# Performance work log

Hardware: AMD Instinct MI355X
Metric: run time of the kernel (lower is better)

Reference implementation:

```python
import jax, jax.numpy as jnp
import numpy as np

N, E, H, K = 2000, 512, 8, 32
DH = E // H  # 64
CLAMP = 10000.0
LN_EPS = 1e-5


def _layernorm(x, g, b):
    mu = jnp.mean(x, axis=-1, keepdims=True)
    var = jnp.mean((x - mu) ** 2, axis=-1, keepdims=True)
    return (x - mu) * jax.lax.rsqrt(var + LN_EPS) * g + b


def setup_inputs() -> dict:
    key = jax.random.key(0)
    ks = jax.random.split(key, 16)
    s_in = 1.0 / np.sqrt(E)
    inp = {
        'x': jax.random.normal(ks[0], (N, E), jnp.float32),
        'coords9': jax.random.normal(ks[1], (N, 9), jnp.float32),
        'prompt_signal': jax.random.normal(ks[2], (E,), jnp.float32),
        # pos_encoder: Linear(3, E//4) + GELU + LayerNorm(E//4)
        'pos_w1': jax.random.normal(ks[3], (E // 4, 3), jnp.float32) * 0.5,
        'pos_b1': jax.random.normal(ks[4], (E // 4,), jnp.float32) * 0.02,
        'pos_ln_g': jnp.ones((E // 4,), jnp.float32),
        'pos_ln_b': jnp.zeros((E // 4,), jnp.float32),
        # MultiheadAttention in/out projections
        'wq': jax.random.normal(ks[5], (E, E), jnp.float32) * s_in,
        'wk': jax.random.normal(ks[6], (E, E), jnp.float32) * s_in,
        'wv': jax.random.normal(ks[7], (E, E), jnp.float32) * s_in,
        'bq': jnp.zeros((E,), jnp.float32),
        'bk': jnp.zeros((E,), jnp.float32),
        'bv': jnp.zeros((E,), jnp.float32),
        'wo': jax.random.normal(ks[8], (E, E), jnp.float32) * s_in,
        'bo': jnp.zeros((E,), jnp.float32),
    }
    return inp


def reference(x, coords9, prompt_signal, pos_w1, pos_b1, pos_ln_g, pos_ln_b,
              wq, wk, wv, bq, bk, bv, wo, bo):
    n = x.shape[0]
    # centroids of triangle faces: (N,3)
    centroids = coords9.reshape(n, 3, 3).mean(axis=1)
    # pairwise centroid distances (only relation feature that affects output)
    diff = centroids[:, None, :] - centroids[None, :, :]        # (N,N,3)
    distances = jnp.linalg.norm(diff, axis=-1)                   # (N,N)
    # positional encoding branch
    pos_enc = _layernorm(jax.nn.gelu(centroids @ pos_w1.T + pos_b1, approximate=False),
                         pos_ln_g, pos_ln_b)                     # (N,E/4)
    prompt_enhanced = x + prompt_signal[None, :]
    pos_enhanced = jnp.concatenate([prompt_enhanced[:, :3 * E // 4], pos_enc], axis=-1)  # (N,E)
    # top-k nearest neighbors mask (k smallest distances per row)
    _, topk_idx = jax.lax.top_k(-distances, K)                   # (N,K)
    attn_mask = jnp.full((n, n), -jnp.inf, jnp.float32)
    attn_mask = attn_mask.at[jnp.arange(n)[:, None], topk_idx].set(0.0)
    # multi-head attention, self q=k=v, fp32
    q = (pos_enhanced @ wq.T + bq).reshape(n, H, DH)
    k = (pos_enhanced @ wk.T + bk).reshape(n, H, DH)
    v = (pos_enhanced @ wv.T + bv).reshape(n, H, DH)
    scores = jnp.einsum('nhd,mhd->hnm', q, k) / np.sqrt(DH) + attn_mask[None]
    attn = jax.nn.softmax(scores, axis=-1)                       # (H,N,N)
    ctx = jnp.einsum('hnm,mhd->nhd', attn, v).reshape(n, E)
    out = ctx @ wo.T + bo
    # _sanitize_tensor
    out = jnp.nan_to_num(out, nan=0.0, posinf=CLAMP, neginf=-CLAMP)
    return jnp.clip(out, -CLAMP, CLAMP)
```

## Files before the change

### kernel.cpp

```cpp
#include <hip/hip_runtime.h>
#include <math.h>

#define NN_K 32
#define E_DIM 512
#define CLAMP_V 10000.0f

typedef __attribute__((ext_vector_type(8))) short short8;
typedef __attribute__((ext_vector_type(4))) float f32x4;

__device__ __forceinline__ unsigned short f2bf(float x) {
  unsigned u = __float_as_uint(x);
  unsigned r = u + 0x7fffu + ((u >> 16) & 1u);
  return (unsigned short)(r >> 16);
}
__device__ __forceinline__ float bf2f_bits(short h) {
  return __uint_as_float(((unsigned)(unsigned short)h) << 16);
}

__device__ __forceinline__ void async16(const void* g, void* l) {
  __builtin_amdgcn_global_load_lds((const __attribute__((address_space(1))) void*)g,
                                   (__attribute__((address_space(3))) void*)l, 16, 0, 0);
}

__global__ __launch_bounds__(256) void front_kernel(
    const float* __restrict__ x, const float* __restrict__ coords9,
    const float* __restrict__ prompt,
    const float* __restrict__ w1, const float* __restrict__ b1,
    const float* __restrict__ ln_g, const float* __restrict__ ln_b,
    const float* __restrict__ wq, const float* __restrict__ wk,
    const float* __restrict__ wv, const float* __restrict__ wo,
    short* __restrict__ w_bf, short* __restrict__ pos_bf,
    int* __restrict__ topk, int N, int Mpad)
{
  int blk = blockIdx.x;
  int t = threadIdx.x;

  if (blk < 256) {
    #pragma unroll
    for (int i = 0; i < 4; ++i) {
      int v = blk * 256 + t + i * 65536;
      int m = v >> 16;
      int e = v & 0xffff;
      const float* src = m == 0 ? wq : (m == 1 ? wk : (m == 2 ? wv : wo));
      float4 f = ((const float4*)src)[e];
      short4 h;
      h.x = (short)f2bf(f.x); h.y = (short)f2bf(f.y);
      h.z = (short)f2bf(f.z); h.w = (short)f2bf(f.w);
      ((short4*)w_bf)[v] = h;
    }
    return;
  }

  if (blk < 2304) {
    int n = blk - 256;
    size_t rb = (size_t)n * E_DIM;
    if (n >= N) {
      #pragma unroll
      for (int j = t; j < E_DIM; j += 256) pos_bf[rb + j] = 0;
      return;
    }
    __shared__ float red[4];
    float g = 0.f;
    if (t < 128) {
      const float* c9 = coords9 + n * 9;
      float c0 = (c9[0] + c9[3] + c9[6]) / 3.0f;
      float c1 = (c9[1] + c9[4] + c9[7]) / 3.0f;
      float c2 = (c9[2] + c9[5] + c9[8]) / 3.0f;
      float pre = c0 * w1[t*3+0] + c1 * w1[t*3+1] + c2 * w1[t*3+2] + b1[t];
      g = 0.5f * pre * (1.0f + erff(pre * 0.70710678118654752440f));
      float s = g;
      #pragma unroll
      for (int o = 32; o > 0; o >>= 1) s += __shfl_xor(s, o);
      if ((t & 63) == 0) red[t >> 6] = s;
    }
    __syncthreads();
    float mu = (red[0] + red[1]) * (1.0f / 128.0f);
    float d = g - mu;
    if (t < 128) {
      float s2 = d * d;
      #pragma unroll
      for (int o = 32; o > 0; o >>= 1) s2 += __shfl_xor(s2, o);
      if ((t & 63) == 0) red[2 + (t >> 6)] = s2;
    }
    __syncthreads();
    if (t < 128) {
      float var = (red[2] + red[3]) * (1.0f / 128.0f);
      float y = d * rsqrtf(var + 1e-5f) * ln_g[t] + ln_b[t];
      pos_bf[rb + 384 + t] = (short)f2bf(y);
    }
    #pragma unroll
    for (int j = t; j < 384; j += 256)
      pos_bf[rb + j] = (short)f2bf(x[rb + j] + prompt[j]);
    return;
  }

  {
    __shared__ unsigned hist[256];
    __shared__ unsigned waveSums[4];
    __shared__ unsigned sel_bin, sel_rem;
    __shared__ unsigned cnt, tcnt;
    __shared__ unsigned tie[2048];

    int n = blk - 2304;
    int lane = t & 63, wid = t >> 6;
    const float* cn = coords9 + n * 9;
    float cx = (cn[0] + cn[3] + cn[6]) / 3.0f;
    float cy = (cn[1] + cn[4] + cn[7]) / 3.0f;
    float cz = (cn[2] + cn[5] + cn[8]) / 3.0f;

    unsigned bits[8];
    #pragma unroll
    for (int r = 0; r < 8; ++r) {
      int m = t + (r << 8);
      unsigned b = 0xFFFFFFFFu;
      if (m < N) {
        const float* cm = coords9 + m * 9;
        float mx_ = (cm[0] + cm[3] + cm[6]) / 3.0f;
        float my_ = (cm[1] + cm[4] + cm[7]) / 3.0f;
        float mz_ = (cm[2] + cm[5] + cm[8]) / 3.0f;
        float dx = cx - mx_, dy = cy - my_, dz = cz - mz_;
        float dist = sqrtf(dx*dx + dy*dy + dz*dz);
        b = __float_as_uint(dist);
      }
      bits[r] = b;
    }

    unsigned prefix = 0;
    unsigned K_rem = NN_K;
    #pragma unroll
    for (int p = 0; p < 4; ++p) {
      int shift = 24 - 8 * p;
      unsigned high_mask = (p == 0) ? 0u : (0xFFFFFFFFu << (8 * (4 - p)));
      hist[t] = 0;
      __syncthreads();
      #pragma unroll
      for (int r = 0; r < 8; ++r) {
        if ((bits[r] & high_mask) == prefix)
          atomicAdd(&hist[(bits[r] >> shift) & 255], 1u);
      }
      __syncthreads();
      unsigned h = hist[t];
      unsigned scan = h;
      #pragma unroll
      for (int o = 1; o < 64; o <<= 1) {
        unsigned u = __shfl_up(scan, o);
        if (lane >= o) scan += u;
      }
      if (lane == 63) waveSums[wid] = scan;
      __syncthreads();
      unsigned off = 0;
      for (int w = 0; w < wid; ++w) off += waveSums[w];
      scan += off;
      if (scan >= K_rem && (scan - h) < K_rem) {
        sel_bin = (unsigned)t;
        sel_rem = K_rem - (scan - h);
      }
      __syncthreads();
      prefix |= sel_bin << shift;
      K_rem = sel_rem;
      __syncthreads();
    }

    unsigned T = prefix;
    if (t == 0) { cnt = 0; tcnt = 0; }
    __syncthreads();
    #pragma unroll
    for (int r = 0; r < 8; ++r) {
      int m = t + (r << 8);
      if (m < N) {
        if (bits[r] < T) {
          unsigned slot = atomicAdd(&cnt, 1u);
          topk[n * NN_K + slot] = m;
        } else if (bits[r] == T) {
          unsigned tp = atomicAdd(&tcnt, 1u);
          tie[tp] = (unsigned)m;
        }
      }
    }
    __syncthreads();
    if (t == 0) {
      unsigned base = cnt;
      unsigned need = K_rem;
      for (unsigned it = 0; it < need; ++it) {
        unsigned best = 0xFFFFFFFFu, bj = 0;
        for (unsigned j = 0; j < tcnt; ++j)
          if (tie[j] < best) { best = tie[j]; bj = j; }
        topk[n * NN_K + base + it] = (int)best;
        tie[bj] = 0xFFFFFFFFu;
      }
    }
  }
}

__device__ __forceinline__ void gemm_core(
    const short* __restrict__ A, const short* __restrict__ W,
    const float* __restrict__ bias,
    float* __restrict__ outf, short* __restrict__ outb,
    int out_ld, int out_c0,
    int M, int row0, int col0, bool doClamp)
{
  __shared__ short sA[2][64 * 32], sB[2][128 * 32];
  int tid = threadIdx.x;
  int cr = tid >> 2;
  int ck = (tid & 3) << 3;
  const short* gA = A + (size_t)(row0 + cr) * 512 + ck;
  const short* gB = W + (size_t)(col0 + cr) * 512 + ck;
  int lo = tid * 8, loB1 = (tid + 256) * 8;
  const size_t rstep = (size_t)64 * 512;

  int lane = tid & 63, wv_ = tid >> 6;
  int wn = wv_ << 5;
  int lr = lane & 15, lq = lane >> 4;

#define STAGE(t, b) do { \
    async16(gA + (t) * 32,         &sA[b][lo]); \
    async16(gB + (t) * 32,         &sB[b][lo]); \
    async16(gB + (t) * 32 + rstep, &sB[b][loB1]); } while (0)

  STAGE(0, 0);
  STAGE(1, 1);

  f32x4 acc[4][2];
  #pragma unroll
  for (int i = 0; i < 4; ++i)
    #pragma unroll
    for (int j = 0; j < 2; ++j)
      acc[i][j] = (f32x4){0.f, 0.f, 0.f, 0.f};

  #pragma unroll
  for (int it = 0; it < 16; ++it) {
    int cur = it & 1;
    if (it == 15) asm volatile("s_waitcnt vmcnt(0)\ns_barrier" ::: "memory");
    else          asm volatile("s_waitcnt vmcnt(3)\ns_barrier" ::: "memory");

    short8 af[4], bf[2];
    #pragma unroll
    for (int i = 0; i < 4; ++i)
      af[i] = *(const short8*)&sA[cur][((i << 4) + lr) * 32 + (lq << 3)];
    #pragma unroll
    for (int j = 0; j < 2; ++j)
      bf[j] = *(const short8*)&sB[cur][(wn + (j << 4) + lr) * 32 + (lq << 3)];
    #pragma unroll
    for (int i = 0; i < 4; ++i)
      #pragma unroll
      for (int j = 0; j < 2; ++j)
        acc[i][j] = __builtin_amdgcn_mfma_f32_16x16x32_bf16(af[i], bf[j], acc[i][j], 0, 0, 0);

    asm volatile("s_waitcnt lgkmcnt(0)\ns_barrier" ::: "memory");
    if (it + 2 < 16) STAGE(it + 2, cur);
  }
#undef STAGE

  #pragma unroll
  for (int j = 0; j < 2; ++j) {
    int gcol = col0 + wn + (j << 4) + lr;
    float bv_ = bias[gcol];
    #pragma unroll
    for (int i = 0; i < 4; ++i) {
      #pragma unroll
      for (int r = 0; r < 4; ++r) {
        int grow = row0 + (i << 4) + (lq << 2) + r;
        if (grow < M) {
          float v = acc[i][j][r] + bv_;
          if (doClamp) {
            v = isnan(v) ? 0.0f : v;
            v = fminf(fmaxf(v, -CLAMP_V), CLAMP_V);
          }
          if (outf) outf[(size_t)grow * 512 + gcol] = v;
          else      outb[(size_t)grow * out_ld + out_c0 + gcol] = (short)f2bf(v);
        }
      }
    }
  }
}

__global__ __launch_bounds__(256) void qkv_mfma(
    const short* __restrict__ A, const short* __restrict__ Wb,
    const float* __restrict__ bq, const float* __restrict__ bk, const float* __restrict__ bv,
    float* __restrict__ qb, short* __restrict__ kv, int M)
{
  int sel = blockIdx.y >> 2;
  int nblk = blockIdx.y & 3;
  int r0 = blockIdx.x * 64, c0 = nblk * 128;
  if (sel == 0)
    gemm_core(A, Wb, bq, qb, nullptr, 512, 0, M, r0, c0, false);
  else if (sel == 1)
    gemm_core(A, Wb + 262144, bk, nullptr, kv, 1024, 0, M, r0, c0, false);
  else
    gemm_core(A, Wb + 2 * 262144, bv, nullptr, kv, 1024, 512, M, r0, c0, false);
}

__global__ __launch_bounds__(256) void out_mfma(
    const short* __restrict__ A, const short* __restrict__ Wb,
    const float* __restrict__ bias, float* __restrict__ out, int M)
{
  gemm_core(A, Wb + (size_t)3 * 262144, bias, out, nullptr, 512, 0, M,
            blockIdx.x * 64, blockIdx.y * 128, true);
}

__global__ __launch_bounds__(512) void attn_kernel(
    const float* __restrict__ qb, const short* __restrict__ kv,
    const int* __restrict__ topk, short* __restrict__ ctx_bf, int N)
{
  __shared__ short klds[32 * 512];
  __shared__ int sidx[NN_K];
  __shared__ float plds[8 * 32];

  int n = blockIdx.x;
  int tid = threadIdx.x;
  size_t rb = (size_t)n * E_DIM;
  if (n >= N) { ctx_bf[rb + tid] = 0; return; }

  if (tid < NN_K) sidx[tid] = topk[n * NN_K + tid];
  __syncthreads();

  int h = tid >> 6, lane = tid & 63;
  int jk = lane & 31, half = lane >> 5;
  int dbase = h * 64 + half * 32;

  float qv[32];
  {
    const float4* qs = (const float4*)(qb + rb + dbase);
    #pragma unroll
    for (int b = 0; b < 8; ++b) {
      float4 f = qs[b];
      qv[b*4+0] = f.x; qv[b*4+1] = f.y; qv[b*4+2] = f.z; qv[b*4+3] = f.w;
    }
  }

  {
    int j = tid >> 4, a = tid & 15;
    const short8* src = (const short8*)(kv + (size_t)sidx[j] * 1024 + a * 32);
    int sw = 4 * (j & 15);
    short* row = &klds[j * 512];
    #pragma unroll
    for (int b = 0; b < 4; ++b) {
      short8 val = src[b];
      int d0 = a * 32 + b * 8;
      *(short4*)&row[(d0    ) ^ sw] = *(const short4*)&val;
      *(short4*)&row[(d0 + 4) ^ sw] = *((const short4*)&val + 1);
    }
  }
  __syncthreads();

  float s = 0.f;
  {
    int sw = 4 * (jk & 15);
    const short* krow = &klds[jk * 512];
    #pragma unroll
    for (int i4 = 0; i4 < 8; ++i4) {
      short4 kkv = *(const short4*)&krow[(dbase + i4 * 4) ^ sw];
      s += qv[i4*4+0] * bf2f_bits(kkv.x) + qv[i4*4+1] * bf2f_bits(kkv.y)
         + qv[i4*4+2] * bf2f_bits(kkv.z) + qv[i4*4+3] * bf2f_bits(kkv.w);
    }
  }
  s += __shfl_xor(s, 32);
  s *= 0.125f;

  float mx = s;
  #pragma unroll
  for (int o = 16; o > 0; o >>= 1) mx = fmaxf(mx, __shfl_xor(mx, o));
  float p = expf(s - mx);
  float l = p;
  #pragma unroll
  for (int o = 16; o > 0; o >>= 1) l += __shfl_xor(l, o);
  p *= (1.0f / l);
  if (half == 0) plds[h * 32 + jk] = p;
  __syncthreads();

  float pv[32];
  #pragma unroll
  for (int b = 0; b < 8; ++b) {
    float4 f = *(const float4*)&plds[h * 32 + b * 4];
    pv[b*4+0] = f.x; pv[b*4+1] = f.y; pv[b*4+2] = f.z; pv[b*4+3] = f.w;
  }

  int off = 512 + h * 64 + lane;
  float acc = 0.f;
  #pragma unroll
  for (int j = 0; j < NN_K; ++j)
    acc += pv[j] * bf2f_bits(kv[(size_t)sidx[j] * 1024 + off]);
  ctx_bf[rb + h * 64 + lane] = (short)f2bf(acc);
}

extern "C" void kernel_launch(void* const* d_in, const int* in_sizes, int n_in,
                              void* d_out, int out_size, void* d_ws, size_t ws_size,
                              hipStream_t stream) {
  const float* x       = (const float*)d_in[0];
  const float* coords9 = (const float*)d_in[1];
  const float* prompt  = (const float*)d_in[2];
  const float* pos_w1  = (const float*)d_in[3];
  const float* pos_b1  = (const float*)d_in[4];
  const float* ln_g    = (const float*)d_in[5];
  const float* ln_b    = (const float*)d_in[6];
  const float* wq      = (const float*)d_in[7];
  const float* wk      = (const float*)d_in[8];
  const float* wv      = (const float*)d_in[9];
  const float* bq      = (const float*)d_in[10];
  const float* bk      = (const float*)d_in[11];
  const float* bv      = (const float*)d_in[12];
  const float* wo      = (const float*)d_in[13];
  const float* bo      = (const float*)d_in[14];

  int N = in_sizes[1] / 9;
  int Mpad = (N + 127) & ~127;
  size_t PE = (size_t)Mpad * E_DIM;

  char* p = (char*)d_ws;
  short* pos_bf = (short*)p; p += PE * 2;
  short* w_bf   = (short*)p; p += (size_t)4 * 512 * 512 * 2;
  float* qb     = (float*)p; p += PE * 4;
  short* kv_bf  = (short*)p; p += PE * 2 * 2;
  short* ctx_bf = (short*)p; p += PE * 2;
  int*   topk   = (int*)p;

  front_kernel<<<256 + Mpad + N, 256, 0, stream>>>(
      x, coords9, prompt, pos_w1, pos_b1, ln_g, ln_b,
      wq, wk, wv, wo, w_bf, pos_bf, topk, N, Mpad);

  dim3 gq(Mpad / 64, 12);
  qkv_mfma<<<gq, 256, 0, stream>>>(pos_bf, w_bf, bq, bk, bv, qb, kv_bf, Mpad);
  attn_kernel<<<Mpad, 512, 0, stream>>>(qb, kv_bf, topk, ctx_bf, N);

  dim3 go(Mpad / 64, 4);
  out_mfma<<<go, 256, 0, stream>>>(ctx_bf, w_bf, bo, (float*)d_out, N);
}
```

Baseline: 154.7 us.

## Move top-k neighbor selection into QKV GEMM launch and precompute centroids

The radix-select top-k blocks move out of the front kernel and into extra grid rows of the QKV GEMM kernel. Top-k now runs concurrently with the projection GEMMs instead of with the weight conversion and layernorm work. The front kernel also writes centroids as float4 once, so top-k reads precomputed centroids instead of recomputing them from coords9. Shared memory is merged into one buffer reused for GEMM staging and the tie list. The cost is larger LDS per block for the GEMM blocks, which may lower occupancy.

```diff
diff --git a/kernel.cpp b/kernel.cpp
--- a/kernel.cpp
+++ b/kernel.cpp
@@ -30,7 +30,7 @@
     const float* __restrict__ wq, const float* __restrict__ wk,
     const float* __restrict__ wv, const float* __restrict__ wo,
     short* __restrict__ w_bf, short* __restrict__ pos_bf,
-    int* __restrict__ topk, int N, int Mpad)
+    float* __restrict__ cent, int N)
 {
   int blk = blockIdx.x;
   int t = threadIdx.x;
@@ -51,155 +51,61 @@
     return;
   }
 
-  if (blk < 2304) {
-    int n = blk - 256;
-    size_t rb = (size_t)n * E_DIM;
-    if (n >= N) {
-      #pragma unroll
-      for (int j = t; j < E_DIM; j += 256) pos_bf[rb + j] = 0;
-      return;
-    }
-    __shared__ float red[4];
-    float g = 0.f;
-    if (t < 128) {
-      const float* c9 = coords9 + n * 9;
-      float c0 = (c9[0] + c9[3] + c9[6]) / 3.0f;
-      float c1 = (c9[1] + c9[4] + c9[7]) / 3.0f;
-      float c2 = (c9[2] + c9[5] + c9[8]) / 3.0f;
-      float pre = c0 * w1[t*3+0] + c1 * w1[t*3+1] + c2 * w1[t*3+2] + b1[t];
-      g = 0.5f * pre * (1.0f + erff(pre * 0.70710678118654752440f));
-      float s = g;
-      #pragma unroll
-      for (int o = 32; o > 0; o >>= 1) s += __shfl_xor(s, o);
-      if ((t & 63) == 0) red[t >> 6] = s;
-    }
-    __syncthreads();
-    float mu = (red[0] + red[1]) * (1.0f / 128.0f);
-    float d = g - mu;
-    if (t < 128) {
-      float s2 = d * d;
-      #pragma unroll
-      for (int o = 32; o > 0; o >>= 1) s2 += __shfl_xor(s2, o);
-      if ((t & 63) == 0) red[2 + (t >> 6)] = s2;
-    }
-    __syncthreads();
-    if (t < 128) {
-      float var = (red[2] + red[3]) * (1.0f / 128.0f);
-      float y = d * rsqrtf(var + 1e-5f) * ln_g[t] + ln_b[t];
-      pos_bf[rb + 384 + t] = (short)f2bf(y);
-    }
-    #pragma unroll
-    for (int j = t; j < 384; j += 256)
-      pos_bf[rb + j] = (short)f2bf(x[rb + j] + prompt[j]);
+  int n = blk - 256;
+  size_t rb = (size_t)n * E_DIM;
+  if (n >= N) {
+    #pragma unroll
+    for (int j = t; j < E_DIM; j += 256) pos_bf[rb + j] = 0;
     return;
   }
-
-  {
-    __shared__ unsigned hist[256];
-    __shared__ unsigned waveSums[4];
-    __shared__ unsigned sel_bin, sel_rem;
-    __shared__ unsigned cnt, tcnt;
-    __shared__ unsigned tie[2048];
-
-    int n = blk - 2304;
-    int lane = t & 63, wid = t >> 6;
-    const float* cn = coords9 + n * 9;
-    float cx = (cn[0] + cn[3] + cn[6]) / 3.0f;
-    float cy = (cn[1] + cn[4] + cn[7]) / 3.0f;
-    float cz = (cn[2] + cn[5] + cn[8]) / 3.0f;
-
-    unsigned bits[8];
-    #pragma unroll
-    for (int r = 0; r < 8; ++r) {
-      int m = t + (r << 8);
-      unsigned b = 0xFFFFFFFFu;
-      if (m < N) {
-        const float* cm = coords9 + m * 9;
-        float mx_ = (cm[0] + cm[3] + cm[6]) / 3.0f;
-        float my_ = (cm[1] + cm[4] + cm[7]) / 3.0f;
-        float mz_ = (cm[2] + cm[5] + cm[8]) / 3.0f;
-        float dx = cx - mx_, dy = cy - my_, dz = cz - mz_;
-        float dist = sqrtf(dx*dx + dy*dy + dz*dz);
-        b = __float_as_uint(dist);
-      }
-      bits[r] = b;
-    }
-
-    unsigned prefix = 0;
-    unsigned K_rem = NN_K;
-    #pragma unroll
-    for (int p = 0; p < 4; ++p) {
-      int shift = 24 - 8 * p;
-      unsigned high_mask = (p == 0) ? 0u : (0xFFFFFFFFu << (8 * (4 - p)));
-      hist[t] = 0;
-      __syncthreads();
-      #pragma unroll
-      for (int r = 0; r < 8; ++r) {
-        if ((bits[r] & high_mask) == prefix)
-          atomicAdd(&hist[(bits[r] >> shift) & 255], 1u);
-      }
-      __syncthreads();
-      unsigned h = hist[t];
-      unsigned scan = h;
-      #pragma unroll
-      for (int o = 1; o < 64; o <<= 1) {
-        unsigned u = __shfl_up(scan, o);
-        if (lane >= o) scan += u;
-      }
-      if (lane == 63) waveSums[wid] = scan;
-      __syncthreads();
-      unsigned off = 0;
-      for (int w = 0; w < wid; ++w) off += waveSums[w];
-      scan += off;
-      if (scan >= K_rem && (scan - h) < K_rem) {
-        sel_bin = (unsigned)t;
-        sel_rem = K_rem - (scan - h);
-      }
-      __syncthreads();
-      prefix |= sel_bin << shift;
-      K_rem = sel_rem;
-      __syncthreads();
-    }
-
-    unsigned T = prefix;
-    if (t == 0) { cnt = 0; tcnt = 0; }
-    __syncthreads();
-    #pragma unroll
-    for (int r = 0; r < 8; ++r) {
-      int m = t + (r << 8);
-      if (m < N) {
-        if (bits[r] < T) {
-          unsigned slot = atomicAdd(&cnt, 1u);
-          topk[n * NN_K + slot] = m;
-        } else if (bits[r] == T) {
-          unsigned tp = atomicAdd(&tcnt, 1u);
-          tie[tp] = (unsigned)m;
-        }
-      }
-    }
-    __syncthreads();
+  __shared__ float red[4];
+  float g = 0.f;
+  if (t < 128) {
+    const float* c9 = coords9 + n * 9;
+    float c0 = (c9[0] + c9[3] + c9[6]) / 3.0f;
+    float c1 = (c9[1] + c9[4] + c9[7]) / 3.0f;
+    float c2 = (c9[2] + c9[5] + c9[8]) / 3.0f;
     if (t == 0) {
-      unsigned base = cnt;
-      unsigned need = K_rem;
-      for (unsigned it = 0; it < need; ++it) {
-        unsigned best = 0xFFFFFFFFu, bj = 0;
-        for (unsigned j = 0; j < tcnt; ++j)
-          if (tie[j] < best) { best = tie[j]; bj = j; }
-        topk[n * NN_K + base + it] = (int)best;
-        tie[bj] = 0xFFFFFFFFu;
-      }
-    }
-  }
+      float4 c; c.x = c0; c.y = c1; c.z = c2; c.w = 0.f;
+      ((float4*)cent)[n] = c;
+    }
+    float pre = c0 * w1[t*3+0] + c1 * w1[t*3+1] + c2 * w1[t*3+2] + b1[t];
+    g = 0.5f * pre * (1.0f + erff(pre * 0.70710678118654752440f));
+    float s = g;
+    #pragma unroll
+    for (int o = 32; o > 0; o >>= 1) s += __shfl_xor(s, o);
+    if ((t & 63) == 0) red[t >> 6] = s;
+  }
+  __syncthreads();
+  float mu = (red[0] + red[1]) * (1.0f / 128.0f);
+  float d = g - mu;
+  if (t < 128) {
+    float s2 = d * d;
+    #pragma unroll
+    for (int o = 32; o > 0; o >>= 1) s2 += __shfl_xor(s2, o);
+    if ((t & 63) == 0) red[2 + (t >> 6)] = s2;
+  }
+  __syncthreads();
+  if (t < 128) {
+    float var = (red[2] + red[3]) * (1.0f / 128.0f);
+    float y = d * rsqrtf(var + 1e-5f) * ln_g[t] + ln_b[t];
+    pos_bf[rb + 384 + t] = (short)f2bf(y);
+  }
+  #pragma unroll
+  for (int j = t; j < 384; j += 256)
+    pos_bf[rb + j] = (short)f2bf(x[rb + j] + prompt[j]);
 }
 
 __device__ __forceinline__ void gemm_core(
+    char* smem,
     const short* __restrict__ A, const short* __restrict__ W,
     const float* __restrict__ bias,
     float* __restrict__ outf, short* __restrict__ outb,
     int out_ld, int out_c0,
     int M, int row0, int col0, bool doClamp)
 {
-  __shared__ short sA[2][64 * 32], sB[2][128 * 32];
+  short* sA = (short*)smem;
+  short* sB = (short*)(smem + 8192);
   int tid = threadIdx.x;
   int cr = tid >> 2;
   int ck = (tid & 3) << 3;
@@ -213,9 +119,9 @@
   int lr = lane & 15, lq = lane >> 4;
 
 #define STAGE(t, b) do { \
-    async16(gA + (t) * 32,         &sA[b][lo]); \
-    async16(gB + (t) * 32,         &sB[b][lo]); \
-    async16(gB + (t) * 32 + rstep, &sB[b][loB1]); } while (0)
+    async16(gA + (t) * 32,         sA + (b) * 2048 + lo); \
+    async16(gB + (t) * 32,         sB + (b) * 4096 + lo); \
+    async16(gB + (t) * 32 + rstep, sB + (b) * 4096 + loB1); } while (0)
 
   STAGE(0, 0);
   STAGE(1, 1);
@@ -236,10 +142,10 @@
     short8 af[4], bf[2];
     #pragma unroll
     for (int i = 0; i < 4; ++i)
-      af[i] = *(const short8*)&sA[cur][((i << 4) + lr) * 32 + (lq << 3)];
+      af[i] = *(const short8*)&sA[cur * 2048 + ((i << 4) + lr) * 32 + (lq << 3)];
     #pragma unroll
     for (int j = 0; j < 2; ++j)
-      bf[j] = *(const short8*)&sB[cur][(wn + (j << 4) + lr) * 32 + (lq << 3)];
+      bf[j] = *(const short8*)&sB[cur * 4096 + (wn + (j << 4) + lr) * 32 + (lq << 3)];
     #pragma unroll
     for (int i = 0; i < 4; ++i)
       #pragma unroll
@@ -274,27 +180,129 @@
   }
 }
 
-__global__ __launch_bounds__(256) void qkv_mfma(
+__global__ __launch_bounds__(256) void qkv_topk(
     const short* __restrict__ A, const short* __restrict__ Wb,
     const float* __restrict__ bq, const float* __restrict__ bk, const float* __restrict__ bv,
-    float* __restrict__ qb, short* __restrict__ kv, int M)
+    float* __restrict__ qb, short* __restrict__ kv,
+    const float* __restrict__ cent, int* __restrict__ topk,
+    int M, int N)
 {
-  int sel = blockIdx.y >> 2;
-  int nblk = blockIdx.y & 3;
-  int r0 = blockIdx.x * 64, c0 = nblk * 128;
-  if (sel == 0)
-    gemm_core(A, Wb, bq, qb, nullptr, 512, 0, M, r0, c0, false);
-  else if (sel == 1)
-    gemm_core(A, Wb + 262144, bk, nullptr, kv, 1024, 0, M, r0, c0, false);
-  else
-    gemm_core(A, Wb + 2 * 262144, bv, nullptr, kv, 1024, 512, M, r0, c0, false);
+  __shared__ __align__(16) char smem[24576];
+  __shared__ unsigned hist[256];
+  __shared__ unsigned waveSums[4];
+  __shared__ unsigned sel_bin, sel_rem;
+  __shared__ unsigned cnt, tcnt;
+
+  int by = blockIdx.y;
+  if (by < 12) {
+    int sel = by >> 2;
+    int nblk = by & 3;
+    int r0 = blockIdx.x * 64, c0 = nblk * 128;
+    if (sel == 0)
+      gemm_core(smem, A, Wb, bq, qb, nullptr, 512, 0, M, r0, c0, false);
+    else if (sel == 1)
+      gemm_core(smem, A, Wb + 262144, bk, nullptr, kv, 1024, 0, M, r0, c0, false);
+    else
+      gemm_core(smem, A, Wb + 2 * 262144, bv, nullptr, kv, 1024, 512, M, r0, c0, false);
+    return;
+  }
+
+  int n = (by - 12) * gridDim.x + blockIdx.x;
+  if (n >= N) return;
+  unsigned* tie = (unsigned*)smem;
+
+  int t = threadIdx.x;
+  int lane = t & 63, wid = t >> 6;
+  const float4* cq = (const float4*)cent;
+  float4 c = cq[n];
+  float cx = c.x, cy = c.y, cz = c.z;
+
+  unsigned bits[8];
+  #pragma unroll
+  for (int r = 0; r < 8; ++r) {
+    int m = t + (r << 8);
+    unsigned b = 0xFFFFFFFFu;
+    if (m < N) {
+      float4 cm = cq[m];
+      float dx = cx - cm.x, dy = cy - cm.y, dz = cz - cm.z;
+      float dist = sqrtf(dx*dx + dy*dy + dz*dz);
+      b = __float_as_uint(dist);
+    }
+    bits[r] = b;
+  }
+
+  unsigned prefix = 0;
+  unsigned K_rem = NN_K;
+  #pragma unroll
+  for (int p = 0; p < 4; ++p) {
+    int shift = 24 - 8 * p;
+    unsigned high_mask = (p == 0) ? 0u : (0xFFFFFFFFu << (8 * (4 - p)));
+    hist[t] = 0;
+    __syncthreads();
+    #pragma unroll
+    for (int r = 0; r < 8; ++r) {
+      if ((bits[r] & high_mask) == prefix)
+        atomicAdd(&hist[(bits[r] >> shift) & 255], 1u);
+    }
+    __syncthreads();
+    unsigned h = hist[t];
+    unsigned scan = h;
+    #pragma unroll
+    for (int o = 1; o < 64; o <<= 1) {
+      unsigned u = __shfl_up(scan, o);
+      if (lane >= o) scan += u;
+    }
+    if (lane == 63) waveSums[wid] = scan;
+    __syncthreads();
+    unsigned off = 0;
+    for (int w = 0; w < wid; ++w) off += waveSums[w];
+    scan += off;
+    if (scan >= K_rem && (scan - h) < K_rem) {
+      sel_bin = (unsigned)t;
+      sel_rem = K_rem - (scan - h);
+    }
+    __syncthreads();
+    prefix |= sel_bin << shift;
+    K_rem = sel_rem;
+    __syncthreads();
+  }
+
+  unsigned T = prefix;
+  if (t == 0) { cnt = 0; tcnt = 0; }
+  __syncthreads();
+  #pragma unroll
+  for (int r = 0; r < 8; ++r) {
+    int m = t + (r << 8);
+    if (m < N) {
+      if (bits[r] < T) {
+        unsigned slot = atomicAdd(&cnt, 1u);
+        topk[n * NN_K + slot] = m;
+      } else if (bits[r] == T) {
+        unsigned tp = atomicAdd(&tcnt, 1u);
+        tie[tp] = (unsigned)m;
+      }
+    }
+  }
+  __syncthreads();
+  if (t == 0) {
+    unsigned base = cnt;
+    unsigned need = K_rem;
+    for (unsigned it = 0; it < need; ++it) {
+      unsigned best = 0xFFFFFFFFu, bj = 0;
+      for (unsigned j = 0; j < tcnt; ++j)
+        if (tie[j] < best) { best = tie[j]; bj = j; }
+      topk[n * NN_K + base + it] = (int)best;
+      tie[bj] = 0xFFFFFFFFu;
+    }
+  }
 }
 
 __global__ __launch_bounds__(256) void out_mfma(
     const short* __restrict__ A, const short* __restrict__ Wb,
     const float* __restrict__ bias, float* __restrict__ out, int M)
 {
-  gemm_core(A, Wb + (size_t)3 * 262144, bias, out, nullptr, 512, 0, M,
+  __shared__ __align__(16) char smem[24576];
+  gemm_core(smem, A, Wb + (size_t)3 * 262144, bias, out, nullptr, 512, 0, M,
             blockIdx.x * 64, blockIdx.y * 128, true);
 }
 
@@ -412,14 +420,17 @@
   float* qb     = (float*)p; p += PE * 4;
   short* kv_bf  = (short*)p; p += PE * 2 * 2;
   short* ctx_bf = (short*)p; p += PE * 2;
-  int*   topk   = (int*)p;
-
-  front_kernel<<<256 + Mpad + N, 256, 0, stream>>>(
+  int*   topk   = (int*)p;   p += (size_t)Mpad * NN_K * 4;
+  float* cent   = (float*)p;
+
+  front_kernel<<<256 + Mpad, 256, 0, stream>>>(
       x, coords9, prompt, pos_w1, pos_b1, ln_g, ln_b,
-      wq, wk, wv, wo, w_bf, pos_bf, topk, N, Mpad);
-
-  dim3 gq(Mpad / 64, 12);
-  qkv_mfma<<<gq, 256, 0, stream>>>(pos_bf, w_bf, bq, bk, bv, qb, kv_bf, Mpad);
+      wq, wk, wv, wo, w_bf, pos_bf, cent, N);
+
+  int gx = Mpad / 64;
+  dim3 gq(gx, 12 + (N + gx - 1) / gx);
+  qkv_topk<<<gq, 256, 0, stream>>>(pos_bf, w_bf, bq, bk, bv, qb, kv_bf,
+                                   cent, topk, Mpad, N);
   attn_kernel<<<Mpad, 512, 0, stream>>>(qb, kv_bf, topk, ctx_bf, N);
 
   dim3 go(Mpad / 64, 4);
```

After: 154.7 us. No clear change (-0.0%).
